# Performance work log

Hardware: AMD Instinct MI355X
Metric: run time of the kernel (lower is better)

## Reference

```python
import jax, jax.numpy as jnp
import numpy as np

LAYER_SIZES = [4096, 8192, 8192, 4096, 1024]
BATCH = 4096
SCARCITY = 0.05


def setup_inputs() -> dict:
    key = jax.random.key(0)
    ks = jax.random.split(key, 5)
    inp = {"x": jax.random.normal(ks[0], (LAYER_SIZES[0], BATCH), dtype=jnp.float32)}
    for i in range(4):
        out_d, in_d = LAYER_SIZES[i + 1], LAYER_SIZES[i]
        # uniform(-0.1, 0.1) mirrors the repo's weight_initialization(a=-0.1, b=0.1)
        inp[f"W{i}"] = jax.random.uniform(ks[i + 1], (out_d, in_d), dtype=jnp.float32,
                                          minval=-0.1, maxval=0.1)
        inp[f"thr{i}"] = jnp.ones((out_d,), dtype=jnp.float32)  # starting_threshold = 1.0
    return inp


def _kwta(x, thr, k):
    # x: [out, batch]; per-column k-winners-take-all on (x - thr)
    act = x - thr[:, None]
    kth = jax.lax.top_k(act.T, k)[0][:, -1]          # [batch] k-th largest per column
    mask = act >= kth[None, :]
    return jnp.where(mask, x, jnp.zeros_like(x))


def reference(x, W0, W1, W2, W3, thr0, thr1, thr2, thr3):
    Ws = [W0, W1, W2, W3]
    thrs = [thr0, thr1, thr2, thr3]
    n_layers = len(Ws)
    for i in range(n_layers):
        x = Ws[i] @ x                                 # [out_i, batch]
        if i < n_layers - 1:
            x = jax.nn.relu(x)
        k = int(SCARCITY * Ws[i].shape[0])
        x = _kwta(x, thrs[i], k)
    return jax.nn.softmax(x, axis=0)                  # output_activation over features
```

## Files before the change

### kernel.cpp

```cpp
#include <hip/hip_runtime.h>

typedef _Float16 f16x8 __attribute__((ext_vector_type(8)));
typedef _Float16 f16x4 __attribute__((ext_vector_type(4)));
typedef float f32x4 __attribute__((ext_vector_type(4)));

#define NB 4096

__device__ __forceinline__ void gload16(const void* g, void* l) {
    __builtin_amdgcn_global_load_lds(
        (const __attribute__((address_space(1))) unsigned int*)g,
        (__attribute__((address_space(3))) unsigned int*)l, 16, 0, 0);
}

__global__ __launch_bounds__(256) void tsplit_kernel(const float* __restrict__ X,
                                                     _Float16* __restrict__ Oh,
                                                     _Float16* __restrict__ Ol) {
    __shared__ float t[64][65];
    const int f0 = blockIdx.x * 64, b0 = blockIdx.y * 64;
    const int tid = threadIdx.x;
    const int jj = tid & 63, i0 = tid >> 6;
#pragma unroll
    for (int p = 0; p < 16; ++p) {
        int i = p * 4 + i0;
        t[i][jj] = X[(size_t)(f0 + i) * NB + b0 + jj];
    }
    __syncthreads();
#pragma unroll
    for (int p = 0; p < 16; ++p) {
        int b = p * 4 + i0;
        float v = t[jj][b];
        size_t idx = (size_t)(b0 + b) * 4096 + f0 + jj;
        _Float16 h = (_Float16)v;
        Oh[idx] = h;
        Ol[idx] = (_Float16)((v - (float)h) * 2048.0f);
    }
}

__global__ __launch_bounds__(256) void splitw_kernel(const float* __restrict__ W,
                                                     _Float16* __restrict__ Wh,
                                                     _Float16* __restrict__ Wl, long n4) {
    long i = (long)blockIdx.x * 256 + threadIdx.x;
    const long stride = (long)gridDim.x * 256;
    for (; i < n4; i += stride) {
        float4 w = ((const float4*)W)[i];
        float vs[4] = {w.x, w.y, w.z, w.w};
        f16x4 h, l;
#pragma unroll
        for (int j = 0; j < 4; ++j) {
            _Float16 hh = (_Float16)vs[j];
            h[j] = hh;
            l[j] = (_Float16)((vs[j] - (float)hh) * 2048.0f);
        }
        ((f16x4*)Wh)[i] = h;
        ((f16x4*)Wl)[i] = l;
    }
}

__global__ __launch_bounds__(512, 2) void gemm3p_kernel(
    const _Float16* __restrict__ Ah, const _Float16* __restrict__ Al,
    const _Float16* __restrict__ Bh, const _Float16* __restrict__ Bl,
    float* __restrict__ C, int K, int M, int do_relu) {
    __shared__ __align__(16) char lds[3][49152];

    const int tid = threadIdx.x;
    const int gx = gridDim.x;
    int bid = blockIdx.y * gx + blockIdx.x;
    const int SC = gx < 16 ? gx : 16;
    const int SR = 256 / SC;
    const int nsc = gx / SC;
    const int s = bid >> 8, w = bid & 255;
    const int col0 = ((s % nsc) * SC + (w % SC)) * 256;
    const int row0 = ((s / nsc) * SR + (w / SC)) * 128;

    const int wid = tid >> 6, lane = tid & 63;
    const int wm = wid >> 2, wn = wid & 3;
    const int lr = lane & 15;
    const int rdoff = (((lane >> 4) ^ ((lane >> 1) & 3)) << 4);

    f32x4 acc[4][4] = {};
    f32x4 accx[4][4] = {};

    const int srow = tid >> 2;
    const int scl = (tid & 3) ^ ((tid >> 3) & 3);
    const size_t sk = (size_t)K;
    const _Float16* gA_h = Ah + (size_t)(row0 + srow) * sk + scl * 8;
    const _Float16* gA_l = Al + (size_t)(row0 + srow) * sk + scl * 8;
    const _Float16* gB_h0 = Bh + (size_t)(col0 + srow) * sk + scl * 8;
    const _Float16* gB_h1 = Bh + (size_t)(col0 + 128 + srow) * sk + scl * 8;
    const _Float16* gB_l0 = Bl + (size_t)(col0 + srow) * sk + scl * 8;
    const _Float16* gB_l1 = Bl + (size_t)(col0 + 128 + srow) * sk + scl * 8;
    const int ldsA = tid * 16;

#define STAGE_G0(Lb, go) { gload16(gA_h + go, (Lb) + ldsA); gload16(gA_l + go, (Lb) + 8192 + ldsA); }
#define STAGE_G1(Lb, go) { gload16(gB_h0 + go, (Lb) + 16384 + ldsA); gload16(gB_h1 + go, (Lb) + 24576 + ldsA); }
#define STAGE_G2(Lb, go) { gload16(gB_l0 + go, (Lb) + 32768 + ldsA); gload16(gB_l1 + go, (Lb) + 40960 + ldsA); }

    const int NT = K / 32;
    {
        STAGE_G0(lds[0], 0); STAGE_G1(lds[0], 0); STAGE_G2(lds[0], 0);
        STAGE_G0(lds[1], 32); STAGE_G1(lds[1], 32); STAGE_G2(lds[1], 32);
    }

    for (int t = 0; t < NT; ++t) {
        if (t < NT - 1) {
            asm volatile("s_waitcnt vmcnt(6)" ::: "memory");
        } else {
            asm volatile("s_waitcnt vmcnt(0)" ::: "memory");
        }
        __builtin_amdgcn_s_barrier();
        asm volatile("" ::: "memory");

        const char* Lb = lds[t % 3];
        char* Ls = lds[(t + 2) % 3];
        const bool do_stage = (t + 2 < NT);
        const size_t go = (size_t)(t + 2) * 32;

        const char* sAh_ = Lb;
        const char* sAl_ = Lb + 8192;
        const char* sBh_ = Lb + 16384;
        const char* sBl_ = Lb + 32768;

        f16x8 ah[4], al[4], bh[4], bl[4];
#pragma unroll
        for (int mi = 0; mi < 4; ++mi) {
            const int ra = wm * 64 + mi * 16 + lr;
            ah[mi] = *(const f16x8*)(sAh_ + ra * 64 + rdoff);
            al[mi] = *(const f16x8*)(sAl_ + ra * 64 + rdoff);
        }
#pragma unroll
        for (int ni = 0; ni < 2; ++ni) {
            const int rb = wn * 64 + ni * 16 + lr;
            bh[ni] = *(const f16x8*)(sBh_ + rb * 64 + rdoff);
            bl[ni] = *(const f16x8*)(sBl_ + rb * 64 + rdoff);
        }
#pragma unroll
        for (int ni = 0; ni < 4; ++ni) {
            if (ni < 3) {
                asm volatile("s_waitcnt lgkmcnt(2)" ::: "memory");
            } else {
                asm volatile("s_waitcnt lgkmcnt(0)" ::: "memory");
            }
            if (ni < 2) {
                const int rb = wn * 64 + (ni + 2) * 16 + lr;
                bh[ni + 2] = *(const f16x8*)(sBh_ + rb * 64 + rdoff);
                bl[ni + 2] = *(const f16x8*)(sBl_ + rb * 64 + rdoff);
            }
            if (do_stage) {
                if (ni == 0) STAGE_G0(Ls, go)
                else if (ni == 1) STAGE_G1(Ls, go)
                else if (ni == 2) STAGE_G2(Ls, go)
            }
            __builtin_amdgcn_sched_barrier(0);
            __builtin_amdgcn_s_setprio(1);
#pragma unroll
            for (int mi = 0; mi < 4; ++mi) {
                acc[mi][ni] = __builtin_amdgcn_mfma_f32_16x16x32_f16(ah[mi], bh[ni], acc[mi][ni], 0, 0, 0);
                accx[mi][ni] = __builtin_amdgcn_mfma_f32_16x16x32_f16(ah[mi], bl[ni], accx[mi][ni], 0, 0, 0);
                accx[mi][ni] = __builtin_amdgcn_mfma_f32_16x16x32_f16(al[mi], bh[ni], accx[mi][ni], 0, 0, 0);
            }
            __builtin_amdgcn_s_setprio(0);
        }
    }
#undef STAGE_G0
#undef STAGE_G1
#undef STAGE_G2

#pragma unroll
    for (int mi = 0; mi < 4; ++mi)
#pragma unroll
        for (int ni = 0; ni < 4; ++ni) {
            int colx = col0 + wn * 64 + ni * 16 + lr;
            int rowb = row0 + wm * 64 + mi * 16 + ((lane >> 4) << 2);
#pragma unroll
            for (int r = 0; r < 4; ++r) {
                float v = acc[mi][ni][r] + accx[mi][ni][r] * (1.0f / 2048.0f);
                if (do_relu) v = fmaxf(v, 0.0f);
                C[(size_t)(rowb + r) * M + colx] = v;
            }
        }
}

__global__ __launch_bounds__(256, 2) void gemm3_kernel(
    const _Float16* __restrict__ Ah, const _Float16* __restrict__ Al,
    const _Float16* __restrict__ Bh, const _Float16* __restrict__ Bl,
    float* __restrict__ C, int K, int M, int do_relu) {
    __shared__ __align__(16) _Float16 sAh[128 * 32];
    __shared__ __align__(16) _Float16 sAl[128 * 32];
    __shared__ __align__(16) _Float16 sBh[128 * 32];
    __shared__ __align__(16) _Float16 sBl[128 * 32];

    const int tid = threadIdx.x;
    const int row0 = blockIdx.y * 128;
    const int col0 = blockIdx.x * 128;
    const int wid = tid >> 6, lane = tid & 63;
    const int wm = wid >> 1, wn = wid & 1;
    const int lr = lane & 15, lk = (lane >> 4) * 8;

    f32x4 acc[4][4] = {};
    f32x4 accx[4][4] = {};

    const int o0 = tid * 16;
    const int o1 = o0 + 4096;
    const int r0 = o0 >> 6, c0 = o0 & 63;
    const int r1 = o1 >> 6, c1 = o1 & 63;
    const size_t sk = (size_t)K * 2;

    const char* gAh0 = (const char*)Ah + (size_t)(row0 + r0) * sk + c0;
    const char* gAh1 = (const char*)Ah + (size_t)(row0 + r1) * sk + c1;
    const char* gAl0 = (const char*)Al + (size_t)(row0 + r0) * sk + c0;
    const char* gAl1 = (const char*)Al + (size_t)(row0 + r1) * sk + c1;
    const char* gBh0 = (const char*)Bh + (size_t)(col0 + r0) * sk + c0;
    const char* gBh1 = (const char*)Bh + (size_t)(col0 + r1) * sk + c1;
    const char* gBl0 = (const char*)Bl + (size_t)(col0 + r0) * sk + c0;
    const char* gBl1 = (const char*)Bl + (size_t)(col0 + r1) * sk + c1;

    for (int k0 = 0; k0 < K; k0 += 32) {
        __syncthreads();
        gload16(gAh0, (char*)sAh + o0);
        gload16(gAh1, (char*)sAh + o1);
        gload16(gAl0, (char*)sAl + o0);
        gload16(gAl1, (char*)sAl + o1);
        gload16(gBh0, (char*)sBh + o0);
        gload16(gBh1, (char*)sBh + o1);
        gload16(gBl0, (char*)sBl + o0);
        gload16(gBl1, (char*)sBl + o1);
        gAh0 += 64; gAh1 += 64; gAl0 += 64; gAl1 += 64;
        gBh0 += 64; gBh1 += 64; gBl0 += 64; gBl1 += 64;
        __syncthreads();

        f16x8 bh[4], bl[4];
#pragma unroll
        for (int ni = 0; ni < 4; ++ni) {
            int rb = wn * 64 + ni * 16 + lr;
            bh[ni] = *(const f16x8*)&sBh[rb * 32 + lk];
            bl[ni] = *(const f16x8*)&sBl[rb * 32 + lk];
        }
#pragma unroll
        for (int mi = 0; mi < 4; ++mi) {
            int ra = wm * 64 + mi * 16 + lr;
            f16x8 ah = *(const f16x8*)&sAh[ra * 32 + lk];
            f16x8 al = *(const f16x8*)&sAl[ra * 32 + lk];
#pragma unroll
            for (int ni = 0; ni < 4; ++ni) {
                acc[mi][ni] = __builtin_amdgcn_mfma_f32_16x16x32_f16(ah, bh[ni], acc[mi][ni], 0, 0, 0);
                accx[mi][ni] = __builtin_amdgcn_mfma_f32_16x16x32_f16(ah, bl[ni], accx[mi][ni], 0, 0, 0);
                accx[mi][ni] = __builtin_amdgcn_mfma_f32_16x16x32_f16(al, bh[ni], accx[mi][ni], 0, 0, 0);
            }
        }
    }
#pragma unroll
    for (int mi = 0; mi < 4; ++mi)
#pragma unroll
        for (int ni = 0; ni < 4; ++ni) {
            int colx = col0 + wn * 64 + ni * 16 + lr;
            int rowb = row0 + wm * 64 + mi * 16 + (lane >> 4) * 4;
#pragma unroll
            for (int r = 0; r < 4; ++r) {
                float v = acc[mi][ni][r] + accx[mi][ni][r] * (1.0f / 2048.0f);
                if (do_relu) v = fmaxf(v, 0.0f);
                C[(size_t)(rowb + r) * M + colx] = v;
            }
        }
}

template <int CNT, bool SOFTMAX>
__global__ __launch_bounds__(256) void kwta_kernel(const float* __restrict__ Cin,
                                                   const float* __restrict__ thr,
                                                   _Float16* __restrict__ Oh,
                                                   _Float16* __restrict__ Ol,
                                                   float* __restrict__ outT, int M, int k) {
    const int row = blockIdx.x, tid = threadIdx.x;
    const float* rp = Cin + (size_t)row * M;
    unsigned uv[CNT];
    float xv[CNT];
#pragma unroll
    for (int i = 0; i < CNT; ++i) {
        int col = i * 256 + tid;
        float x = rp[col];
        float a = x - thr[col];
        unsigned b = __float_as_uint(a);
        uv[i] = (b & 0x80000000u) ? ~b : (b | 0x80000000u);
        xv[i] = x;
    }
    __shared__ int hist[256];
    __shared__ unsigned sel_s;
    __shared__ int kk_s;
    unsigned prefix = 0;
    int kk = k;
#pragma unroll
    for (int pass = 0; pass < 4; ++pass) {
        const int shift = 24 - pass * 8;
        hist[tid] = 0;
        __syncthreads();
#pragma unroll
        for (int i = 0; i < CNT; ++i) {
            bool ok = (pass == 0) || ((uv[i] >> (shift + 8)) == prefix);
            if (ok) atomicAdd(&hist[(uv[i] >> shift) & 255], 1);
        }
        __syncthreads();
        for (int off = 1; off < 256; off <<= 1) {
            int v = hist[tid] + ((tid + off < 256) ? hist[tid + off] : 0);
            __syncthreads();
            hist[tid] = v;
            __syncthreads();
        }
        if (hist[tid] >= kk && (tid == 255 || hist[tid + 1] < kk)) {
            sel_s = (unsigned)tid;
            kk_s = kk - ((tid == 255) ? 0 : hist[tid + 1]);
        }
        __syncthreads();
        prefix = (prefix << 8) | sel_s;
        kk = kk_s;
        __syncthreads();
    }
    const unsigned kth = prefix;
    if (!SOFTMAX) {
#pragma unroll
        for (int i = 0; i < CNT; ++i) {
            int col = i * 256 + tid;
            float v = (uv[i] >= kth) ? xv[i] : 0.0f;
            size_t idx = (size_t)row * M + col;
            _Float16 h = (_Float16)v;
            Oh[idx] = h;
            Ol[idx] = (_Float16)((v - (float)h) * 2048.0f);
        }
    } else {
        float vals[CNT];
        float m = -3.4e38f;
#pragma unroll
        for (int i = 0; i < CNT; ++i) {
            float v = (uv[i] >= kth) ? xv[i] : 0.0f;
            vals[i] = v;
            m = fmaxf(m, v);
        }
        for (int off = 32; off; off >>= 1) m = fmaxf(m, __shfl_xor(m, off));
        __shared__ float redm[4];
        if ((tid & 63) == 0) redm[tid >> 6] = m;
        __syncthreads();
        m = fmaxf(fmaxf(redm[0], redm[1]), fmaxf(redm[2], redm[3]));
        float s = 0.0f, e[CNT];
#pragma unroll
        for (int i = 0; i < CNT; ++i) {
            e[i] = expf(vals[i] - m);
            s += e[i];
        }
        for (int off = 32; off; off >>= 1) s += __shfl_xor(s, off);
        __shared__ float reds[4];
        if ((tid & 63) == 0) reds[tid >> 6] = s;
        __syncthreads();
        s = reds[0] + reds[1] + reds[2] + reds[3];
        float inv = 1.0f / s;
#pragma unroll
        for (int i = 0; i < CNT; ++i)
            outT[(size_t)(i * 256 + tid) * NB + row] = e[i] * inv;
    }
}

extern "C" void kernel_launch(void* const* d_in, const int* in_sizes, int n_in,
                              void* d_out, int out_size, void* d_ws, size_t ws_size,
                              hipStream_t stream) {
    const float* x = (const float*)d_in[0];
    const float* W0 = (const float*)d_in[1];
    const float* thr0 = (const float*)d_in[2];
    const float* W1 = (const float*)d_in[3];
    const float* thr1 = (const float*)d_in[4];
    const float* W2 = (const float*)d_in[5];
    const float* thr2 = (const float*)d_in[6];
    const float* W3 = (const float*)d_in[7];
    const float* thr3 = (const float*)d_in[8];
    float* out = (float*)d_out;

    char* ws = (char*)d_ws;
    size_t off = 0;
    auto alloc = [&](size_t bytes) {
        void* p = ws + off;
        off += (bytes + 255) & ~(size_t)255;
        return p;
    };
    _Float16* Wh = (_Float16*)alloc((size_t)8192 * 8192 * 2);
    _Float16* Wl = (_Float16*)alloc((size_t)8192 * 8192 * 2);
    _Float16* Xh = (_Float16*)alloc((size_t)4096 * 8192 * 2);
    _Float16* Xl = (_Float16*)alloc((size_t)4096 * 8192 * 2);
    _Float16* Yh = (_Float16*)alloc((size_t)4096 * 8192 * 2);
    _Float16* Yl = (_Float16*)alloc((size_t)4096 * 8192 * 2);
    float* C32 = (float*)alloc((size_t)4096 * 8192 * 4);

    tsplit_kernel<<<dim3(64, 64), 256, 0, stream>>>(x, Xh, Xl);

    splitw_kernel<<<4096, 256, 0, stream>>>(W0, Wh, Wl, (long)8192 * 4096 / 4);
    gemm3p_kernel<<<dim3(8192 / 256, NB / 128), 512, 0, stream>>>(Xh, Xl, Wh, Wl, C32, 4096, 8192, 1);
    kwta_kernel<32, false><<<NB, 256, 0, stream>>>(C32, thr0, Yh, Yl, nullptr, 8192, 409);

    splitw_kernel<<<4096, 256, 0, stream>>>(W1, Wh, Wl, (long)8192 * 8192 / 4);
    gemm3p_kernel<<<dim3(8192 / 256, NB / 128), 512, 0, stream>>>(Yh, Yl, Wh, Wl, C32, 8192, 8192, 1);
    kwta_kernel<32, false><<<NB, 256, 0, stream>>>(C32, thr1, Xh, Xl, nullptr, 8192, 409);

    splitw_kernel<<<4096, 256, 0, stream>>>(W2, Wh, Wl, (long)4096 * 8192 / 4);
    gemm3p_kernel<<<dim3(4096 / 256, NB / 128), 512, 0, stream>>>(Xh, Xl, Wh, Wl, C32, 8192, 4096, 1);
    kwta_kernel<16, false><<<NB, 256, 0, stream>>>(C32, thr2, Yh, Yl, nullptr, 4096, 204);

    splitw_kernel<<<4096, 256, 0, stream>>>(W3, Wh, Wl, (long)1024 * 4096 / 4);
    gemm3_kernel<<<dim3(1024 / 128, NB / 128), 256, 0, stream>>>(Yh, Yl, Wh, Wl, C32, 4096, 1024, 0);
    kwta_kernel<4, true><<<NB, 256, 0, stream>>>(C32, thr3, nullptr, nullptr, out, 1024, 51);
}
```

Baseline: 3.293 ms.

## Reorder gemm3p LDS reads into diagonal wavefront and use it for last layer

Restructures the inner loop of the pipelined split-fp16 GEMM so LDS fragment reads for A and B are issued in pairs, with MFMAs grouped by anti-diagonal. Compute can then start after the first two fragments arrive and later reads overlap earlier MFMAs. It also removes the simpler non-pipelined gemm3 kernel and runs the final 1024-wide layer through gemm3p. That layer's grid is small (4x32 blocks of 512 threads), so it risks lower occupancy or poorer tail balance.

```diff
diff --git a/kernel.cpp b/kernel.cpp
--- a/kernel.cpp
+++ b/kernel.cpp
@@ -121,45 +121,53 @@
         const char* sBl_ = Lb + 32768;
 
         f16x8 ah[4], al[4], bh[4], bl[4];
-#pragma unroll
-        for (int mi = 0; mi < 4; ++mi) {
-            const int ra = wm * 64 + mi * 16 + lr;
-            ah[mi] = *(const f16x8*)(sAh_ + ra * 64 + rdoff);
-            al[mi] = *(const f16x8*)(sAl_ + ra * 64 + rdoff);
-        }
-#pragma unroll
-        for (int ni = 0; ni < 2; ++ni) {
-            const int rb = wn * 64 + ni * 16 + lr;
-            bh[ni] = *(const f16x8*)(sBh_ + rb * 64 + rdoff);
-            bl[ni] = *(const f16x8*)(sBl_ + rb * 64 + rdoff);
-        }
-#pragma unroll
-        for (int ni = 0; ni < 4; ++ni) {
-            if (ni < 3) {
-                asm volatile("s_waitcnt lgkmcnt(2)" ::: "memory");
-            } else {
-                asm volatile("s_waitcnt lgkmcnt(0)" ::: "memory");
-            }
-            if (ni < 2) {
-                const int rb = wn * 64 + (ni + 2) * 16 + lr;
-                bh[ni + 2] = *(const f16x8*)(sBh_ + rb * 64 + rdoff);
-                bl[ni + 2] = *(const f16x8*)(sBl_ + rb * 64 + rdoff);
-            }
-            if (do_stage) {
-                if (ni == 0) STAGE_G0(Ls, go)
-                else if (ni == 1) STAGE_G1(Ls, go)
-                else if (ni == 2) STAGE_G2(Ls, go)
-            }
-            __builtin_amdgcn_sched_barrier(0);
-            __builtin_amdgcn_s_setprio(1);
-#pragma unroll
-            for (int mi = 0; mi < 4; ++mi) {
-                acc[mi][ni] = __builtin_amdgcn_mfma_f32_16x16x32_f16(ah[mi], bh[ni], acc[mi][ni], 0, 0, 0);
-                accx[mi][ni] = __builtin_amdgcn_mfma_f32_16x16x32_f16(ah[mi], bl[ni], accx[mi][ni], 0, 0, 0);
-                accx[mi][ni] = __builtin_amdgcn_mfma_f32_16x16x32_f16(al[mi], bh[ni], accx[mi][ni], 0, 0, 0);
-            }
-            __builtin_amdgcn_s_setprio(0);
-        }
+#define READG(i)                                                              \
+    {                                                                         \
+        const int ra = wm * 64 + (i)*16 + lr;                                 \
+        const int rb = wn * 64 + (i)*16 + lr;                                 \
+        ah[i] = *(const f16x8*)(sAh_ + ra * 64 + rdoff);                      \
+        al[i] = *(const f16x8*)(sAl_ + ra * 64 + rdoff);                      \
+        bh[i] = *(const f16x8*)(sBh_ + rb * 64 + rdoff);                      \
+        bl[i] = *(const f16x8*)(sBl_ + rb * 64 + rdoff);                      \
+    }
+#define CL(mi, ni)                                                                               \
+    {                                                                                            \
+        acc[mi][ni] = __builtin_amdgcn_mfma_f32_16x16x32_f16(ah[mi], bh[ni], acc[mi][ni], 0, 0, 0);  \
+        accx[mi][ni] = __builtin_amdgcn_mfma_f32_16x16x32_f16(ah[mi], bl[ni], accx[mi][ni], 0, 0, 0); \
+        accx[mi][ni] = __builtin_amdgcn_mfma_f32_16x16x32_f16(al[mi], bh[ni], accx[mi][ni], 0, 0, 0); \
+    }
+        READG(0)
+        READG(1)
+        asm volatile("s_waitcnt lgkmcnt(4)" ::: "memory");
+        __builtin_amdgcn_sched_barrier(0);
+        __builtin_amdgcn_s_setprio(1);
+        CL(0, 0)
+        __builtin_amdgcn_s_setprio(0);
+
+        READG(2)
+        if (do_stage) STAGE_G0(Ls, go);
+        asm volatile("s_waitcnt lgkmcnt(4)" ::: "memory");
+        __builtin_amdgcn_sched_barrier(0);
+        __builtin_amdgcn_s_setprio(1);
+        CL(0, 1) CL(1, 0) CL(1, 1)
+        __builtin_amdgcn_s_setprio(0);
+
+        READG(3)
+        if (do_stage) STAGE_G1(Ls, go);
+        asm volatile("s_waitcnt lgkmcnt(4)" ::: "memory");
+        __builtin_amdgcn_sched_barrier(0);
+        __builtin_amdgcn_s_setprio(1);
+        CL(0, 2) CL(1, 2) CL(2, 0) CL(2, 1) CL(2, 2)
+        __builtin_amdgcn_s_setprio(0);
+
+        if (do_stage) STAGE_G2(Ls, go);
+        asm volatile("s_waitcnt lgkmcnt(0)" ::: "memory");
+        __builtin_amdgcn_sched_barrier(0);
+        __builtin_amdgcn_s_setprio(1);
+        CL(0, 3) CL(1, 3) CL(2, 3) CL(3, 0) CL(3, 1) CL(3, 2) CL(3, 3)
+        __builtin_amdgcn_s_setprio(0);
+#undef READG
+#undef CL
     }
 #undef STAGE_G0
 #undef STAGE_G1
@@ -171,89 +179,6 @@
         for (int ni = 0; ni < 4; ++ni) {
             int colx = col0 + wn * 64 + ni * 16 + lr;
             int rowb = row0 + wm * 64 + mi * 16 + ((lane >> 4) << 2);
-#pragma unroll
-            for (int r = 0; r < 4; ++r) {
-                float v = acc[mi][ni][r] + accx[mi][ni][r] * (1.0f / 2048.0f);
-                if (do_relu) v = fmaxf(v, 0.0f);
-                C[(size_t)(rowb + r) * M + colx] = v;
-            }
-        }
-}
-
-__global__ __launch_bounds__(256, 2) void gemm3_kernel(
-    const _Float16* __restrict__ Ah, const _Float16* __restrict__ Al,
-    const _Float16* __restrict__ Bh, const _Float16* __restrict__ Bl,
-    float* __restrict__ C, int K, int M, int do_relu) {
-    __shared__ __align__(16) _Float16 sAh[128 * 32];
-    __shared__ __align__(16) _Float16 sAl[128 * 32];
-    __shared__ __align__(16) _Float16 sBh[128 * 32];
-    __shared__ __align__(16) _Float16 sBl[128 * 32];
-
-    const int tid = threadIdx.x;
-    const int row0 = blockIdx.y * 128;
-    const int col0 = blockIdx.x * 128;
-    const int wid = tid >> 6, lane = tid & 63;
-    const int wm = wid >> 1, wn = wid & 1;
-    const int lr = lane & 15, lk = (lane >> 4) * 8;
-
-    f32x4 acc[4][4] = {};
-    f32x4 accx[4][4] = {};
-
-    const int o0 = tid * 16;
-    const int o1 = o0 + 4096;
-    const int r0 = o0 >> 6, c0 = o0 & 63;
-    const int r1 = o1 >> 6, c1 = o1 & 63;
-    const size_t sk = (size_t)K * 2;
-
-    const char* gAh0 = (const char*)Ah + (size_t)(row0 + r0) * sk + c0;
-    const char* gAh1 = (const char*)Ah + (size_t)(row0 + r1) * sk + c1;
-    const char* gAl0 = (const char*)Al + (size_t)(row0 + r0) * sk + c0;
-    const char* gAl1 = (const char*)Al + (size_t)(row0 + r1) * sk + c1;
-    const char* gBh0 = (const char*)Bh + (size_t)(col0 + r0) * sk + c0;
-    const char* gBh1 = (const char*)Bh + (size_t)(col0 + r1) * sk + c1;
-    const char* gBl0 = (const char*)Bl + (size_t)(col0 + r0) * sk + c0;
-    const char* gBl1 = (const char*)Bl + (size_t)(col0 + r1) * sk + c1;
-
-    for (int k0 = 0; k0 < K; k0 += 32) {
-        __syncthreads();
-        gload16(gAh0, (char*)sAh + o0);
-        gload16(gAh1, (char*)sAh + o1);
-        gload16(gAl0, (char*)sAl + o0);
-        gload16(gAl1, (char*)sAl + o1);
-        gload16(gBh0, (char*)sBh + o0);
-        gload16(gBh1, (char*)sBh + o1);
-        gload16(gBl0, (char*)sBl + o0);
-        gload16(gBl1, (char*)sBl + o1);
-        gAh0 += 64; gAh1 += 64; gAl0 += 64; gAl1 += 64;
-        gBh0 += 64; gBh1 += 64; gBl0 += 64; gBl1 += 64;
-        __syncthreads();
-
-        f16x8 bh[4], bl[4];
-#pragma unroll
-        for (int ni = 0; ni < 4; ++ni) {
-            int rb = wn * 64 + ni * 16 + lr;
-            bh[ni] = *(const f16x8*)&sBh[rb * 32 + lk];
-            bl[ni] = *(const f16x8*)&sBl[rb * 32 + lk];
-        }
-#pragma unroll
-        for (int mi = 0; mi < 4; ++mi) {
-            int ra = wm * 64 + mi * 16 + lr;
-            f16x8 ah = *(const f16x8*)&sAh[ra * 32 + lk];
-            f16x8 al = *(const f16x8*)&sAl[ra * 32 + lk];
-#pragma unroll
-            for (int ni = 0; ni < 4; ++ni) {
-                acc[mi][ni] = __builtin_amdgcn_mfma_f32_16x16x32_f16(ah, bh[ni], acc[mi][ni], 0, 0, 0);
-                accx[mi][ni] = __builtin_amdgcn_mfma_f32_16x16x32_f16(ah, bl[ni], accx[mi][ni], 0, 0, 0);
-                accx[mi][ni] = __builtin_amdgcn_mfma_f32_16x16x32_f16(al, bh[ni], accx[mi][ni], 0, 0, 0);
-            }
-        }
-    }
-#pragma unroll
-    for (int mi = 0; mi < 4; ++mi)
-#pragma unroll
-        for (int ni = 0; ni < 4; ++ni) {
-            int colx = col0 + wn * 64 + ni * 16 + lr;
-            int rowb = row0 + wm * 64 + mi * 16 + (lane >> 4) * 4;
 #pragma unroll
             for (int r = 0; r < 4; ++r) {
                 float v = acc[mi][ni][r] + accx[mi][ni][r] * (1.0f / 2048.0f);
@@ -400,6 +325,6 @@
     kwta_kernel<16, false><<<NB, 256, 0, stream>>>(C32, thr2, Yh, Yl, nullptr, 4096, 204);
 
     splitw_kernel<<<4096, 256, 0, stream>>>(W3, Wh, Wl, (long)1024 * 4096 / 4);
-    gemm3_kernel<<<dim3(1024 / 128, NB / 128), 256, 0, stream>>>(Yh, Yl, Wh, Wl, C32, 4096, 1024, 0);
+    gemm3p_kernel<<<dim3(1024 / 256, NB / 128), 512, 0, stream>>>(Yh, Yl, Wh, Wl, C32, 4096, 1024, 0);
     kwta_kernel<4, true><<<NB, 256, 0, stream>>>(C32, thr3, nullptr, nullptr, out, 1024, 51);
 }
```

After: 3.256 ms (median of 2 runs). Within noise of the previous version (-1.1%).
